# Kernel optimization log

Hardware: AMD Instinct MI355X
Metric: run time of the kernel (lower is better)

## Reference

```python
import jax, jax.numpy as jnp
import numpy as np

B, S, NK, H, D, DM = 2, 2048, 32, 8, 64, 512
NEG = -1e9


def setup_inputs() -> dict:
    key = jax.random.key(0)
    ks = jax.random.split(key, 12)
    hidden_states = jax.random.normal(ks[0], (B, S, DM), jnp.float32)
    rpe = jax.random.normal(ks[1], (B, S, NK, H), jnp.float32)
    idx = jax.random.randint(ks[2], (S, NK), 0, S)
    pad = jax.random.uniform(ks[3], (S, NK)) < 0.1
    q_k_mask = jnp.where(pad, -1, idx).astype(jnp.int32)
    k_q_mask = jax.random.randint(ks[4], (S, NK), 0, S).astype(jnp.int32)  # only used by TVM backward
    sc = 0.02
    w_q = jax.random.normal(ks[5], (DM, H * D), jnp.float32) * sc
    w_k = jax.random.normal(ks[6], (DM, H * D), jnp.float32) * sc
    w_v = jax.random.normal(ks[7], (DM, H * D), jnp.float32) * sc
    fc_w = jax.random.normal(ks[8], (H * D, DM), jnp.float32) * sc
    fc_b = jnp.zeros((DM,), jnp.float32)
    ln_g = jnp.ones((DM,), jnp.float32)
    ln_b = jnp.zeros((DM,), jnp.float32)
    return {"hidden_states": hidden_states, "rpe": rpe, "q_k_mask": q_k_mask,
            "k_q_mask": k_q_mask, "w_q": w_q, "w_k": w_k, "w_v": w_v,
            "fc_w": fc_w, "fc_b": fc_b, "ln_g": ln_g, "ln_b": ln_b}


def reference(hidden_states, rpe, q_k_mask, k_q_mask, w_q, w_k, w_v, fc_w, fc_b, ln_g, ln_b):
    bsz, seq_len, _ = hidden_states.shape
    q = (hidden_states @ w_q).reshape(bsz, seq_len, H, D)
    k = (hidden_states @ w_k).reshape(bsz, seq_len, H, D)
    v = (hidden_states @ w_v).reshape(bsz, seq_len, H, D)

    valid = q_k_mask >= 0                      # [S, NK]
    idx = jnp.where(valid, q_k_mask, 0)        # safe gather index
    vmask = valid[None, :, None, :]            # [1,S,1,NK] broadcast over (b, h)

    # QKP_mm_tvm: sparse QK^T over neighbor lists, plus relative-position bias,
    # padded slots -> -1e9.  k_g: [B,S,NK,H,D]
    k_g = k[:, idx]
    scores = jnp.einsum('bshd,bsnhd->bshn', q, k_g) + rpe.transpose(0, 1, 3, 2)
    scores = jnp.where(vmask, scores, NEG)
    scores = scores / (D ** 0.5)

    attn = jax.nn.softmax(scores, axis=-1)
    # AttnV_mm_tvm with padding 0: padded slots contribute nothing.
    attn = attn * vmask
    v_g = v[:, idx]                            # [B,S,NK,H,D]
    ctx = jnp.einsum('bshn,bsnhd->bshd', attn, v_g).reshape(bsz, seq_len, H * D)

    out = ctx @ fc_w + fc_b + hidden_states    # dropout = identity (eval)
    mu = jnp.mean(out, axis=-1, keepdims=True)
    var = jnp.mean((out - mu) ** 2, axis=-1, keepdims=True)
    return (out - mu) * jax.lax.rsqrt(var + 1e-6) * ln_g + ln_b
```

## Files before the change

kernel.cpp:

```cpp
#include <hip/hip_runtime.h>
#include <hip/hip_bf16.h>

constexpr int Bb  = 2;
constexpr int Ss  = 2048;
constexpr int NKk = 32;
constexpr int Hh  = 8;
constexpr int DMm = 512;
constexpr int Mm  = Bb * Ss;
constexpr int QKV = 1536;

typedef __attribute__((ext_vector_type(8))) short bf16x8;
typedef __attribute__((ext_vector_type(4))) float f32x4;

__device__ __forceinline__ float b2f(unsigned short u) {
  return __uint_as_float((unsigned)u << 16);
}
__device__ __forceinline__ unsigned short f2b(float f) {
  unsigned u = __float_as_uint(f);
  unsigned r = (u + 0x7fffu + ((u >> 16) & 1u)) >> 16;
  return (unsigned short)r;
}
__device__ __forceinline__ void gload_lds16(const ushort* g, ushort* l) {
  __builtin_amdgcn_global_load_lds(
      (const __attribute__((address_space(1))) void*)g,
      (__attribute__((address_space(3))) void*)l, 16, 0, 0);
}

__global__ __launch_bounds__(256) void cvt_bf16_k(
    const float* __restrict__ x, ushort* __restrict__ y, int n8)
{
  const int i = blockIdx.x * 256 + threadIdx.x;
  if (i >= n8) return;
  const float4 a = reinterpret_cast<const float4*>(x)[2 * i];
  const float4 b = reinterpret_cast<const float4*>(x)[2 * i + 1];
  ushort o[8] = {f2b(a.x), f2b(a.y), f2b(a.z), f2b(a.w),
                 f2b(b.x), f2b(b.y), f2b(b.z), f2b(b.w)};
  reinterpret_cast<uint4*>(y)[i] = *reinterpret_cast<uint4*>(o);
}

__global__ __launch_bounds__(256) void cvt_wt_k(
    const float* __restrict__ Wq, const float* __restrict__ Wk,
    const float* __restrict__ Wv, const float* __restrict__ Wf,
    ushort* __restrict__ Wt3, ushort* __restrict__ Wtf)
{
  __shared__ float tile[64][65];
  const int z = blockIdx.z;
  const float* W = (z == 0) ? Wq : (z == 1) ? Wk : (z == 2) ? Wv : Wf;
  ushort* Wt = (z < 3) ? (Wt3 + (size_t)z * 512 * 512) : Wtf;

  const int k0 = blockIdx.x * 64, n0 = blockIdx.y * 64;
  const int t = threadIdx.x;
#pragma unroll
  for (int p = 0; p < 4; ++p) {
    const int r = (t >> 4) + p * 16, c = (t & 15) * 4;
    const float4 v = *reinterpret_cast<const float4*>(&W[(size_t)(k0 + r) * 512 + n0 + c]);
    tile[r][c] = v.x; tile[r][c + 1] = v.y; tile[r][c + 2] = v.z; tile[r][c + 3] = v.w;
  }
  __syncthreads();
  const int n = t >> 2, ks = (t & 3) * 16;
  ushort o[16];
#pragma unroll
  for (int i = 0; i < 16; ++i) o[i] = f2b(tile[ks + i][n]);
  *reinterpret_cast<uint4*>(&Wt[(size_t)(n0 + n) * 512 + k0 + ks])     = *reinterpret_cast<uint4*>(&o[0]);
  *reinterpret_cast<uint4*>(&Wt[(size_t)(n0 + n) * 512 + k0 + ks + 8]) = *reinterpret_cast<uint4*>(&o[8]);
}

template <int OUT_BF16, int BNv>
__global__ __launch_bounds__(256) void gemm_mfma2(
    const ushort* __restrict__ Xb, const ushort* __restrict__ Wt,
    void* __restrict__ Yv, const float* __restrict__ bias,
    const float* __restrict__ resid, int ldY)
{
  constexpr int NJ = BNv / 32;
  constexpr int SMSZ = 8192 + BNv * 64;
  __shared__ ushort smem[SMSZ];
  ushort* As = smem;
  ushort* Bs = smem + 8192;

  const int bm = blockIdx.x * 128;
  const int bn = blockIdx.y * BNv;
  const int t  = threadIdx.x;
  const int wave = t >> 6, lane = t & 63;
  const int wm = (wave >> 1) * 64;
  const int wn = (wave & 1) * (BNv / 2);

  f32x4 acc[4][NJ] = {};

  for (int k0 = 0; k0 < 512; k0 += 64) {
#pragma unroll
    for (int p = 0; p < 4; ++p) {
      const int i = p * 256 + t;
      const int row = i >> 3, sb = i & 7;
      const ushort* g = Xb + (size_t)(bm + row) * 512 + k0 + ((sb ^ (row & 7)) << 3);
      gload_lds16(g, &As[(size_t)(p * 256 + wave * 64) * 8]);
    }
#pragma unroll
    for (int p = 0; p < NJ; ++p) {
      const int i = p * 256 + t;
      const int row = i >> 3, sb = i & 7;
      const ushort* g = Wt + (size_t)(bn + row) * 512 + k0 + ((sb ^ (row & 7)) << 3);
      gload_lds16(g, &Bs[(size_t)(p * 256 + wave * 64) * 8]);
    }
    __syncthreads();
#pragma unroll
    for (int ks = 0; ks < 2; ++ks) {
      const int kb = ks * 4 + (lane >> 4);
      bf16x8 af[4], bfr[NJ];
#pragma unroll
      for (int i = 0; i < 4; ++i) {
        const int row = wm + i * 16 + (lane & 15);
        af[i] = *reinterpret_cast<const bf16x8*>(&As[row * 64 + ((kb ^ (row & 7)) << 3)]);
      }
#pragma unroll
      for (int j = 0; j < NJ; ++j) {
        const int row = wn + j * 16 + (lane & 15);
        bfr[j] = *reinterpret_cast<const bf16x8*>(&Bs[row * 64 + ((kb ^ (row & 7)) << 3)]);
      }
#pragma unroll
      for (int i = 0; i < 4; ++i)
#pragma unroll
        for (int j = 0; j < NJ; ++j)
          acc[i][j] = __builtin_amdgcn_mfma_f32_16x16x32_bf16(af[i], bfr[j], acc[i][j], 0, 0, 0);
    }
    __syncthreads();
  }

  if (OUT_BF16) {
#pragma unroll
    for (int i = 0; i < 4; ++i)
#pragma unroll
      for (int j = 0; j < NJ; ++j)
#pragma unroll
        for (int r = 0; r < 4; ++r) {
          const int row = wm + i * 16 + (lane >> 4) * 4 + r;
          const int col = wn + j * 16 + (lane & 15);
          smem[row * BNv + col] = f2b(acc[i][j][r]);
        }
    __syncthreads();
    ushort* Y = reinterpret_cast<ushort*>(Yv);
    constexpr int CPT = 128 * BNv / 8 / 256;
#pragma unroll
    for (int p = 0; p < CPT; ++p) {
      const int c = p * 256 + t;
      const int row = c / (BNv / 8);
      const int cb  = c % (BNv / 8);
      *reinterpret_cast<uint4*>(&Y[(size_t)(bm + row) * ldY + bn + cb * 8]) =
          *reinterpret_cast<uint4*>(&smem[row * BNv + cb * 8]);
    }
  } else {
    float* Y = reinterpret_cast<float*>(Yv);
#pragma unroll
    for (int i = 0; i < 4; ++i) {
#pragma unroll
      for (int j = 0; j < NJ; ++j) {
        const int m = bm + wm + i * 16 + (lane >> 4) * 4;
        const int n = bn + wn + j * 16 + (lane & 15);
        const float bb = bias[n];
#pragma unroll
        for (int r = 0; r < 4; ++r)
          Y[(size_t)(m + r) * ldY + n] = acc[i][j][r] + bb + resid[(size_t)(m + r) * 512 + n];
      }
    }
  }
}

__global__ __launch_bounds__(256) void attn_k3(
    const ushort* __restrict__ qkv, const float* __restrict__ rpe,
    const int* __restrict__ qkm, ushort* __restrict__ ctx)
{
  __shared__ ushort Ks[32 * 512];
  __shared__ float  qs[512];

  const int bs = blockIdx.x;
  const int b  = bs >> 11;
  const int s  = bs & 2047;
  const int t  = threadIdx.x;
  const int wv = t >> 6, lane = t & 63;

  const ushort* qrow = qkv + (size_t)bs * QKV;
  qs[t]       = b2f(qrow[t]);
  qs[t + 256] = b2f(qrow[t + 256]);

#pragma unroll
  for (int r = 0; r < 8; ++r) {
    const int n = r * 4 + wv;
    int im = qkm[s * NKk + n];
    im = im < 0 ? 0 : im;
    const ushort* gsrc = qkv + (size_t)(b * Ss + im) * QKV + 512
                       + ((lane ^ (n & 7)) * 8);
    gload_lds16(gsrc, &Ks[n * 512]);
  }

  int iv = qkm[s * NKk + (lane & 31)];

  __syncthreads();

  const int h = t >> 5;
  const int n = t & 31;
  const bool valid = (iv >= 0);

  float2 a2 = make_float2(0.f, 0.f);
#pragma unroll
  for (int j = 0; j < 8; ++j) {
    const int blk = (h * 8 + j) ^ (n & 7);
    const uint4 kk = *reinterpret_cast<const uint4*>(&Ks[n * 512 + blk * 8]);
    const float* qq = &qs[h * 64 + j * 8];
    a2.x += qq[0] * __uint_as_float(kk.x << 16);
    a2.y += qq[1] * __uint_as_float(kk.x & 0xffff0000u);
    a2.x += qq[2] * __uint_as_float(kk.y << 16);
    a2.y += qq[3] * __uint_as_float(kk.y & 0xffff0000u);
    a2.x += qq[4] * __uint_as_float(kk.z << 16);
    a2.y += qq[5] * __uint_as_float(kk.z & 0xffff0000u);
    a2.x += qq[6] * __uint_as_float(kk.w << 16);
    a2.y += qq[7] * __uint_as_float(kk.w & 0xffff0000u);
  }
  float sc = a2.x + a2.y + rpe[((size_t)bs * NKk + n) * Hh + h];
  sc = valid ? sc * 0.125f : -1e30f;

  float mx = sc;
#pragma unroll
  for (int m = 16; m >= 1; m >>= 1) mx = fmaxf(mx, __shfl_xor(mx, m, 32));
  const float p = valid ? __expf(sc - mx) : 0.f;
  float sum = p;
#pragma unroll
  for (int m = 16; m >= 1; m >>= 1) sum += __shfl_xor(sum, m, 32);
  const float pn = (sum > 0.f) ? (p / sum) : 0.f;

  const ushort* vbase = qkv + (size_t)b * Ss * QKV + 1024;
  const int e = 2 * t;
  float c0 = 0.f, c1 = 0.f;
#pragma unroll
  for (int n2 = 0; n2 < 32; ++n2) {
    const int src = (lane & 32) + n2;
    const float a = __shfl(pn, src, 64);
    int row = __shfl(iv, src, 64);
    row = row < 0 ? 0 : row;
    const uint vvu = *reinterpret_cast<const uint*>(
        &vbase[(size_t)row * QKV + (e & 511)]);
    c0 += a * __uint_as_float(vvu << 16);
    c1 += a * __uint_as_float(vvu & 0xffff0000u);
  }
  const uint packed = (uint)f2b(c0) | ((uint)f2b(c1) << 16);
  *reinterpret_cast<uint*>(&ctx[(size_t)bs * 512 + e]) = packed;
}

__global__ __launch_bounds__(256) void ln_k(
    float* __restrict__ x, const float* __restrict__ g,
    const float* __restrict__ bta)
{
  const int w    = threadIdx.x >> 6;
  const int lane = threadIdx.x & 63;
  const int row  = blockIdx.x * 4 + w;

  float4* xr = reinterpret_cast<float4*>(x + (size_t)row * 512);
  const float4 v0 = xr[lane];
  const float4 v1 = xr[lane + 64];

  float sum = v0.x + v0.y + v0.z + v0.w + v1.x + v1.y + v1.z + v1.w;
  float sq  = v0.x * v0.x + v0.y * v0.y + v0.z * v0.z + v0.w * v0.w
            + v1.x * v1.x + v1.y * v1.y + v1.z * v1.z + v1.w * v1.w;
#pragma unroll
  for (int m = 32; m >= 1; m >>= 1) {
    sum += __shfl_xor(sum, m, 64);
    sq  += __shfl_xor(sq,  m, 64);
  }
  const float mu  = sum * (1.f / 512.f);
  const float var = sq * (1.f / 512.f) - mu * mu;
  const float rs  = rsqrtf(var + 1e-6f);

  const float4 g0 = reinterpret_cast<const float4*>(g)[lane];
  const float4 g1 = reinterpret_cast<const float4*>(g)[lane + 64];
  const float4 b0 = reinterpret_cast<const float4*>(bta)[lane];
  const float4 b1 = reinterpret_cast<const float4*>(bta)[lane + 64];

  float4 o0, o1;
  o0.x = (v0.x - mu) * rs * g0.x + b0.x;
  o0.y = (v0.y - mu) * rs * g0.y + b0.y;
  o0.z = (v0.z - mu) * rs * g0.z + b0.z;
  o0.w = (v0.w - mu) * rs * g0.w + b0.w;
  o1.x = (v1.x - mu) * rs * g1.x + b1.x;
  o1.y = (v1.y - mu) * rs * g1.y + b1.y;
  o1.z = (v1.z - mu) * rs * g1.z + b1.z;
  o1.w = (v1.w - mu) * rs * g1.w + b1.w;
  xr[lane]      = o0;
  xr[lane + 64] = o1;
}

extern "C" void kernel_launch(void* const* d_in, const int* in_sizes, int n_in,
                              void* d_out, int out_size, void* d_ws, size_t ws_size,
                              hipStream_t stream) {
  const float* hs  = (const float*)d_in[0];
  const float* rpe = (const float*)d_in[1];
  const int*   qkm = (const int*)d_in[2];
  const float* wq  = (const float*)d_in[4];
  const float* wk  = (const float*)d_in[5];
  const float* wv  = (const float*)d_in[6];
  const float* fcw = (const float*)d_in[7];
  const float* fcb = (const float*)d_in[8];
  const float* lng = (const float*)d_in[9];
  const float* lnb = (const float*)d_in[10];
  float* out = (float*)d_out;

  ushort* Xb  = (ushort*)d_ws;
  ushort* Wt3 = Xb  + (size_t)Mm * DMm;
  ushort* Wtf = Wt3 + (size_t)3 * DMm * DMm;
  ushort* qkv = Wtf + (size_t)DMm * DMm;
  ushort* cxb = qkv + (size_t)Mm * QKV;

  cvt_bf16_k<<<(Mm * DMm / 8 + 255) / 256, 256, 0, stream>>>(hs, Xb, Mm * DMm / 8);
  cvt_wt_k<<<dim3(8, 8, 4), 256, 0, stream>>>(wq, wk, wv, fcw, Wt3, Wtf);

  gemm_mfma2<1, 128><<<dim3(Mm / 128, QKV / 128), 256, 0, stream>>>(
      Xb, Wt3, qkv, nullptr, nullptr, QKV);

  attn_k3<<<Mm, 256, 0, stream>>>(qkv, rpe, qkm, cxb);

  gemm_mfma2<0, 64><<<dim3(Mm / 128, DMm / 64), 256, 0, stream>>>(
      cxb, Wtf, out, fcb, hs, DMm);
  ln_k<<<Mm / 4, 256, 0, stream>>>(out, lng, lnb);
}
```

Baseline: 63.57 us.

## Double-buffer GEMM LDS tiles, merge conversion kernels, and retile QKV GEMM

The bf16 GEMM now uses two LDS buffers: it issues async global-to-LDS loads for the next K tile while running MFMAs on the current one, so there is one barrier per step instead of two. The activation and weight conversion kernels are merged into one launch, using extra grid z-slices for the hidden-state cast. The QKV GEMM tile width changes from 128 to 96 columns, which gives more blocks. The costs are more LDS per block, which may lower occupancy, and a 96-wide tile that is less regular for the MFMA layout.

```diff
diff --git a/kernel.cpp b/kernel.cpp
--- a/kernel.cpp
+++ b/kernel.cpp
@@ -26,30 +26,35 @@
       (__attribute__((address_space(3))) void*)l, 16, 0, 0);
 }
 
-__global__ __launch_bounds__(256) void cvt_bf16_k(
-    const float* __restrict__ x, ushort* __restrict__ y, int n8)
-{
-  const int i = blockIdx.x * 256 + threadIdx.x;
-  if (i >= n8) return;
-  const float4 a = reinterpret_cast<const float4*>(x)[2 * i];
-  const float4 b = reinterpret_cast<const float4*>(x)[2 * i + 1];
-  ushort o[8] = {f2b(a.x), f2b(a.y), f2b(a.z), f2b(a.w),
-                 f2b(b.x), f2b(b.y), f2b(b.z), f2b(b.w)};
-  reinterpret_cast<uint4*>(y)[i] = *reinterpret_cast<uint4*>(o);
-}
-
-__global__ __launch_bounds__(256) void cvt_wt_k(
+__global__ __launch_bounds__(256) void cvt_all_k(
+    const float* __restrict__ hs,
     const float* __restrict__ Wq, const float* __restrict__ Wk,
     const float* __restrict__ Wv, const float* __restrict__ Wf,
-    ushort* __restrict__ Wt3, ushort* __restrict__ Wtf)
+    ushort* __restrict__ Xb, ushort* __restrict__ Wt3, ushort* __restrict__ Wtf)
 {
   __shared__ float tile[64][65];
   const int z = blockIdx.z;
+  const int t = threadIdx.x;
+
+  if (z >= 4) {
+    const int cid = (z - 4) * 64 + blockIdx.x * 8 + blockIdx.y;
+    const size_t base8 = (size_t)cid * 1024;
+#pragma unroll
+    for (int it = 0; it < 4; ++it) {
+      const size_t i = base8 + it * 256 + t;
+      const float4 a = reinterpret_cast<const float4*>(hs)[2 * i];
+      const float4 b = reinterpret_cast<const float4*>(hs)[2 * i + 1];
+      ushort o[8] = {f2b(a.x), f2b(a.y), f2b(a.z), f2b(a.w),
+                     f2b(b.x), f2b(b.y), f2b(b.z), f2b(b.w)};
+      reinterpret_cast<uint4*>(Xb)[i] = *reinterpret_cast<uint4*>(o);
+    }
+    return;
+  }
+
   const float* W = (z == 0) ? Wq : (z == 1) ? Wk : (z == 2) ? Wv : Wf;
   ushort* Wt = (z < 3) ? (Wt3 + (size_t)z * 512 * 512) : Wtf;
 
   const int k0 = blockIdx.x * 64, n0 = blockIdx.y * 64;
-  const int t = threadIdx.x;
 #pragma unroll
   for (int p = 0; p < 4; ++p) {
     const int r = (t >> 4) + p * 16, c = (t & 15) * 4;
@@ -66,16 +71,13 @@
 }
 
 template <int OUT_BF16, int BNv>
-__global__ __launch_bounds__(256) void gemm_mfma2(
+__global__ __launch_bounds__(256) void gemm_dbuf(
     const ushort* __restrict__ Xb, const ushort* __restrict__ Wt,
     void* __restrict__ Yv, const float* __restrict__ bias,
     const float* __restrict__ resid, int ldY)
 {
   constexpr int NJ = BNv / 32;
-  constexpr int SMSZ = 8192 + BNv * 64;
-  __shared__ ushort smem[SMSZ];
-  ushort* As = smem;
-  ushort* Bs = smem + 8192;
+  __shared__ ushort smem[16384 + 2 * BNv * 64];
 
   const int bm = blockIdx.x * 128;
   const int bn = blockIdx.y * BNv;
@@ -86,22 +88,28 @@
 
   f32x4 acc[4][NJ] = {};
 
-  for (int k0 = 0; k0 < 512; k0 += 64) {
+  auto stage = [&](int buf, int k0) {
+    ushort* A = smem + buf * 8192;
+    ushort* B = smem + 16384 + buf * (BNv * 64);
 #pragma unroll
     for (int p = 0; p < 4; ++p) {
       const int i = p * 256 + t;
       const int row = i >> 3, sb = i & 7;
-      const ushort* g = Xb + (size_t)(bm + row) * 512 + k0 + ((sb ^ (row & 7)) << 3);
-      gload_lds16(g, &As[(size_t)(p * 256 + wave * 64) * 8]);
+      gload_lds16(Xb + (size_t)(bm + row) * 512 + k0 + ((sb ^ (row & 7)) << 3),
+                  &A[(size_t)(p * 256 + wave * 64) * 8]);
     }
 #pragma unroll
     for (int p = 0; p < NJ; ++p) {
       const int i = p * 256 + t;
       const int row = i >> 3, sb = i & 7;
-      const ushort* g = Wt + (size_t)(bn + row) * 512 + k0 + ((sb ^ (row & 7)) << 3);
-      gload_lds16(g, &Bs[(size_t)(p * 256 + wave * 64) * 8]);
-    }
-    __syncthreads();
+      gload_lds16(Wt + (size_t)(bn + row) * 512 + k0 + ((sb ^ (row & 7)) << 3),
+                  &B[(size_t)(p * 256 + wave * 64) * 8]);
+    }
+  };
+
+  auto compute = [&](int buf) {
+    const ushort* A = smem + buf * 8192;
+    const ushort* B = smem + 16384 + buf * (BNv * 64);
 #pragma unroll
     for (int ks = 0; ks < 2; ++ks) {
       const int kb = ks * 4 + (lane >> 4);
@@ -109,12 +117,12 @@
 #pragma unroll
       for (int i = 0; i < 4; ++i) {
         const int row = wm + i * 16 + (lane & 15);
-        af[i] = *reinterpret_cast<const bf16x8*>(&As[row * 64 + ((kb ^ (row & 7)) << 3)]);
+        af[i] = *reinterpret_cast<const bf16x8*>(&A[row * 64 + ((kb ^ (row & 7)) << 3)]);
       }
 #pragma unroll
       for (int j = 0; j < NJ; ++j) {
         const int row = wn + j * 16 + (lane & 15);
-        bfr[j] = *reinterpret_cast<const bf16x8*>(&Bs[row * 64 + ((kb ^ (row & 7)) << 3)]);
+        bfr[j] = *reinterpret_cast<const bf16x8*>(&B[row * 64 + ((kb ^ (row & 7)) << 3)]);
       }
 #pragma unroll
       for (int i = 0; i < 4; ++i)
@@ -122,10 +130,21 @@
         for (int j = 0; j < NJ; ++j)
           acc[i][j] = __builtin_amdgcn_mfma_f32_16x16x32_bf16(af[i], bfr[j], acc[i][j], 0, 0, 0);
     }
+  };
+
+  stage(0, 0);
+  __syncthreads();
+  int cur = 0;
+  for (int k0 = 64; k0 < 512; k0 += 64) {
+    stage(cur ^ 1, k0);
+    compute(cur);
     __syncthreads();
-  }
+    cur ^= 1;
+  }
+  compute(cur);
 
   if (OUT_BF16) {
+    __syncthreads();
 #pragma unroll
     for (int i = 0; i < 4; ++i)
 #pragma unroll
@@ -307,15 +326,14 @@
   ushort* qkv = Wtf + (size_t)DMm * DMm;
   ushort* cxb = qkv + (size_t)Mm * QKV;
 
-  cvt_bf16_k<<<(Mm * DMm / 8 + 255) / 256, 256, 0, stream>>>(hs, Xb, Mm * DMm / 8);
-  cvt_wt_k<<<dim3(8, 8, 4), 256, 0, stream>>>(wq, wk, wv, fcw, Wt3, Wtf);
-
-  gemm_mfma2<1, 128><<<dim3(Mm / 128, QKV / 128), 256, 0, stream>>>(
+  cvt_all_k<<<dim3(8, 8, 8), 256, 0, stream>>>(hs, wq, wk, wv, fcw, Xb, Wt3, Wtf);
+
+  gemm_dbuf<1, 96><<<dim3(Mm / 128, QKV / 96), 256, 0, stream>>>(
       Xb, Wt3, qkv, nullptr, nullptr, QKV);
 
   attn_k3<<<Mm, 256, 0, stream>>>(qkv, rpe, qkm, cxb);
 
-  gemm_mfma2<0, 64><<<dim3(Mm / 128, DMm / 64), 256, 0, stream>>>(
+  gemm_dbuf<0, 64><<<dim3(Mm / 128, DMm / 64), 256, 0, stream>>>(
       cxb, Wtf, out, fcb, hs, DMm);
   ln_k<<<Mm / 4, 256, 0, stream>>>(out, lng, lnb);
 }
```

Measured after the change: 54.97 us. -13.5%, faster.
